# Kernel optimization log

Measured on AMD Instinct MI355X. Metric: run time of the kernel, lower is better.

## Reference

```python
import jax, jax.numpy as jnp
import numpy as np
from jax import lax

E, H, I, K, T = 16, 2048, 1408, 2, 8192


def setup_inputs() -> dict:
    key = jax.random.key(0)
    k1, k2, k3, k4, k5 = jax.random.split(key, 5)
    hidden_states = jax.random.normal(k1, (T, H), dtype=jnp.float32)
    top_k_index = jax.random.randint(k2, (T, K), 0, E, dtype=jnp.int64)
    top_k_weights = jax.random.uniform(k3, (T, K), dtype=jnp.float32)
    gate_up_proj = jax.random.normal(k4, (E, 2 * I, H), dtype=jnp.float32) * 0.02
    down_proj = jax.random.normal(k5, (E, H, I), dtype=jnp.float32) * 0.02
    return {
        "hidden_states": hidden_states,
        "top_k_index": top_k_index,
        "top_k_weights": top_k_weights,
        "gate_up_proj": gate_up_proj,
        "down_proj": down_proj,
    }


def _moe_forward(hidden_states, top_k_index, top_k_weights, gate_up_proj, down_proj):
    # Combine weight per (expert, token): sum over top-k slots where the slot
    # routes to that expert. Tokens not routed to an expert get weight 0, so the
    # dense per-expert GEMM below computes the exact same math as the gather/
    # scatter-add loop in the original module (masking is linear post-GEMM).
    one_hot = jax.nn.one_hot(top_k_index, E, dtype=top_k_weights.dtype)  # [T,K,E]
    combine = jnp.einsum("tke,tk->et", one_hot, top_k_weights)           # [E,T]

    def expert_step(acc, xs):
        w_gu, w_d, cw = xs                      # [2I,H], [H,I], [T]
        gu = hidden_states @ w_gu.T             # [T,2I]
        gate, up = jnp.split(gu, 2, axis=-1)    # chunk(2, dim=-1)
        h = jax.nn.silu(gate) * up              # SwiGLU
        out = h @ w_d.T                         # [T,H]
        return acc + out * cw[:, None], None

    acc0 = jnp.zeros_like(hidden_states)
    final, _ = lax.scan(expert_step, acc0, (gate_up_proj, down_proj, combine))
    return final


def reference(hidden_states, top_k_index, top_k_weights, gate_up_proj, down_proj):
    return _moe_forward(hidden_states, top_k_index, top_k_weights, gate_up_proj, down_proj)
```

## Files before the change

### kernel.cpp

```cpp
#include <hip/hip_runtime.h>
#include <hip/hip_bf16.h>

#define E_ 16
#define H_ 2048
#define I_ 1408
#define TWOI_ 2816
#define K_ 2
#define T_ 8192
#define TK_ 16384

typedef unsigned short ushort_t;
typedef unsigned int uint_t;
typedef short short8 __attribute__((ext_vector_type(8)));
typedef float f32x4 __attribute__((ext_vector_type(4)));

#define AS1 __attribute__((address_space(1)))
#define AS3 __attribute__((address_space(3)))

__device__ __forceinline__ void gl2lds16(const ushort_t* g, ushort_t* l) {
    __builtin_amdgcn_global_load_lds((const AS1 uint_t*)g, (AS3 uint_t*)l, 16, 0, 0);
}

__device__ __forceinline__ ushort_t f2bf(float f) {
    uint_t u = __float_as_uint(f);
    u += 0x7fffu + ((u >> 16) & 1u);
    return (ushort_t)(u >> 16);
}
__device__ __forceinline__ uint_t pack2(float a, float b) {
    return (uint_t)f2bf(a) | ((uint_t)f2bf(b) << 16);
}
__device__ __forceinline__ float bflo(uint_t v) { return __uint_as_float(v << 16); }
__device__ __forceinline__ float bfhi(uint_t v) { return __uint_as_float(v & 0xffff0000u); }

__global__ void routing_kernel(const int* __restrict__ idx32,
                               const float* __restrict__ wts,
                               int* __restrict__ meta,
                               int* __restrict__ token_ids,
                               float* __restrict__ slot_w) {
    __shared__ int s_cnt[E_], s_off[E_ + 1], s_cur[E_], s_orodd;
    const int tid = threadIdx.x;
    if (tid < E_) { s_cnt[tid] = 0; s_cur[tid] = 0; }
    if (tid == 0) s_orodd = 0;
    __syncthreads();
    int ao = 0;
    for (int s = tid; s < TK_ / 2; s += (int)blockDim.x) ao |= idx32[2 * s + 1];
    atomicOr(&s_orodd, ao);
    __syncthreads();
    const bool is64 = (s_orodd == 0);
    for (int s = tid; s < TK_; s += (int)blockDim.x) {
        int e = is64 ? idx32[2 * s] : idx32[s];
        atomicAdd(&s_cnt[e], 1);
    }
    __syncthreads();
    if (tid == 0) {
        int acc = 0, nt = 0;
        for (int e = 0; e < E_; e++) {
            s_off[e] = acc;
            meta[1 + e] = acc;
            for (int m = 0; m < s_cnt[e]; m += 128) {
                meta[32 + nt] = e;
                meta[192 + nt] = acc + m;
                nt++;
            }
            acc += s_cnt[e];
        }
        s_off[E_] = acc;
        meta[1 + E_] = acc;
        meta[0] = nt;
    }
    __syncthreads();
    for (int s = tid; s < TK_; s += (int)blockDim.x) {
        int e = is64 ? idx32[2 * s] : idx32[s];
        int p = atomicAdd(&s_cur[e], 1);
        int r = s_off[e] + p;
        token_ids[r] = s >> 1;
        slot_w[r] = wts[s];
    }
}

__global__ void f2bf_kernel(const float* __restrict__ src, ushort_t* __restrict__ dst, int n8) {
    int i = blockIdx.x * blockDim.x + threadIdx.x;
    const int stride = gridDim.x * blockDim.x;
    for (; i < n8; i += stride) {
        const float4* s = (const float4*)src + 2 * (size_t)i;
        float4 a = s[0], b = s[1];
        uint4 o;
        o.x = pack2(a.x, a.y);
        o.y = pack2(a.z, a.w);
        o.z = pack2(b.x, b.y);
        o.w = pack2(b.z, b.w);
        ((uint4*)dst)[i] = o;
    }
}

__global__ void swiglu_kernel(const ushort_t* __restrict__ GU, ushort_t* __restrict__ Hb) {
    const int n8 = TK_ * (I_ / 8);
    int i = blockIdx.x * blockDim.x + threadIdx.x;
    const int stride = gridDim.x * blockDim.x;
    for (; i < n8; i += stride) {
        int r = i / (I_ / 8);
        int c = (i % (I_ / 8)) * 8;
        const uint4 gv = *(const uint4*)(GU + (size_t)r * TWOI_ + c);
        const uint4 uv = *(const uint4*)(GU + (size_t)r * TWOI_ + I_ + c);
        const uint_t gs[4] = {gv.x, gv.y, gv.z, gv.w};
        const uint_t us[4] = {uv.x, uv.y, uv.z, uv.w};
        uint_t o[4];
#pragma unroll
        for (int j = 0; j < 4; j++) {
            float g0 = bflo(gs[j]), g1 = bfhi(gs[j]);
            float u0 = bflo(us[j]), u1 = bfhi(us[j]);
            float h0 = g0 / (1.f + __expf(-g0)) * u0;
            float h1 = g1 / (1.f + __expf(-g1)) * u1;
            o[j] = pack2(h0, h1);
        }
        *(uint4*)(Hb + (size_t)r * I_ + c) = make_uint4(o[0], o[1], o[2], o[3]);
    }
}

template <int NCOLS, int KDIM, int MODE>
__global__ __launch_bounds__(256) void moe_gemm(
    const ushort_t* __restrict__ A, const ushort_t* __restrict__ Bw,
    const int* __restrict__ meta, const int* __restrict__ token_ids,
    const float* __restrict__ slot_w, ushort_t* __restrict__ GU,
    float* __restrict__ Out) {
    __shared__ ushort_t As[128 * 32];
    __shared__ ushort_t Bs[128 * 32];
    const int bx = blockIdx.x;
    if (bx >= meta[0]) return;
    const int e = meta[32 + bx];
    const int row0 = meta[192 + bx];
    const int rend = meta[1 + e + 1];
    const int mrows = min(128, rend - row0);
    const int n0 = blockIdx.y * 128;
    const int tid = threadIdx.x;
    const int lane = tid & 63, wid = tid >> 6;
    const int wr = wid >> 1, wc = wid & 1;

    const int c0 = wid * 2, c1 = wid * 2 + 1;
    const int ra0 = c0 * 16 + (lane >> 2);
    const int ra1 = c1 * 16 + (lane >> 2);
    const int kc = (lane & 3) * 8;
    const int rg0 = row0 + min(ra0, mrows - 1);
    const int rg1 = row0 + min(ra1, mrows - 1);
    const long arow0 = (MODE == 0) ? (long)token_ids[rg0] : (long)rg0;
    const long arow1 = (MODE == 0) ? (long)token_ids[rg1] : (long)rg1;
    const ushort_t* ap0 = A + arow0 * KDIM + kc;
    const ushort_t* ap1 = A + arow1 * KDIM + kc;
    const ushort_t* Be = Bw + (size_t)e * NCOLS * KDIM;
    const ushort_t* bp0 = Be + (size_t)(n0 + ra0) * KDIM + kc;
    const ushort_t* bp1 = Be + (size_t)(n0 + ra1) * KDIM + kc;
    ushort_t* as0 = As + c0 * 512;
    ushort_t* as1 = As + c1 * 512;
    ushort_t* bs0 = Bs + c0 * 512;
    ushort_t* bs1 = Bs + c1 * 512;

    f32x4 acc[4][4];
#pragma unroll
    for (int i = 0; i < 4; i++)
#pragma unroll
        for (int j = 0; j < 4; j++) acc[i][j] = (f32x4){0.f, 0.f, 0.f, 0.f};

    for (int k = 0; k < KDIM; k += 32) {
        __syncthreads();
        gl2lds16(ap0, as0);
        gl2lds16(ap1, as1);
        gl2lds16(bp0, bs0);
        gl2lds16(bp1, bs1);
        ap0 += 32; ap1 += 32; bp0 += 32; bp1 += 32;
        __syncthreads();
        short8 af[4], bf[4];
        const int fr = lane & 15, fq = (lane >> 4) * 8;
#pragma unroll
        for (int mt = 0; mt < 4; mt++)
            af[mt] = *(const short8*)(As + (wr * 64 + mt * 16 + fr) * 32 + fq);
#pragma unroll
        for (int nt = 0; nt < 4; nt++)
            bf[nt] = *(const short8*)(Bs + (wc * 64 + nt * 16 + fr) * 32 + fq);
#pragma unroll
        for (int mt = 0; mt < 4; mt++)
#pragma unroll
            for (int nt = 0; nt < 4; nt++)
                acc[mt][nt] = __builtin_amdgcn_mfma_f32_16x16x32_bf16(af[mt], bf[nt], acc[mt][nt], 0, 0, 0);
    }

    const int quad = lane >> 4, tn = lane & 15;
    if (MODE == 0) {
#pragma unroll
        for (int mt = 0; mt < 4; mt++) {
#pragma unroll
            for (int reg = 0; reg < 4; reg++) {
                const int rl = wr * 64 + mt * 16 + quad * 4 + reg;
                if (rl < mrows) {
                    ushort_t* dst = GU + (size_t)(row0 + rl) * NCOLS + n0 + wc * 64 + tn;
#pragma unroll
                    for (int nt = 0; nt < 4; nt++) dst[nt * 16] = f2bf(acc[mt][nt][reg]);
                }
            }
        }
    } else {
#pragma unroll
        for (int mt = 0; mt < 4; mt++) {
#pragma unroll
            for (int reg = 0; reg < 4; reg++) {
                const int rl = wr * 64 + mt * 16 + quad * 4 + reg;
                if (rl < mrows) {
                    const int row = row0 + rl;
                    const int t = token_ids[row];
                    const float w = slot_w[row];
                    float* dst = Out + (size_t)t * NCOLS + n0 + wc * 64 + tn;
#pragma unroll
                    for (int nt = 0; nt < 4; nt++) atomicAdd(dst + nt * 16, acc[mt][nt][reg] * w);
                }
            }
        }
    }
}

extern "C" void kernel_launch(void* const* d_in, const int* in_sizes, int n_in,
                              void* d_out, int out_size, void* d_ws, size_t ws_size,
                              hipStream_t stream) {
    const float* hidden = (const float*)d_in[0];
    const int* topk_idx = (const int*)d_in[1];
    const float* topk_w = (const float*)d_in[2];
    const float* w_gu = (const float*)d_in[3];
    const float* w_d = (const float*)d_in[4];
    float* out = (float*)d_out;

    char* ws = (char*)d_ws;
    int* meta = (int*)ws;
    int* token_ids = (int*)(ws + 4096);
    float* slot_w = (float*)(ws + 4096 + 65536);
    ushort_t* Xb = (ushort_t*)(ws + 135168);
    ushort_t* Wgu = Xb + (size_t)T_ * H_;
    ushort_t* Wd = Wgu + (size_t)E_ * TWOI_ * H_;
    ushort_t* GU = Wd + (size_t)E_ * H_ * I_;
    ushort_t* Hb = GU + (size_t)TK_ * TWOI_;

    hipMemsetAsync(d_out, 0, (size_t)out_size * sizeof(float), stream);

    routing_kernel<<<1, 1024, 0, stream>>>(topk_idx, topk_w, meta, token_ids, slot_w);

    f2bf_kernel<<<4096, 256, 0, stream>>>(hidden, Xb, (int)((size_t)T_ * H_ / 8));
    f2bf_kernel<<<8192, 256, 0, stream>>>(w_gu, Wgu, (int)((size_t)E_ * TWOI_ * H_ / 8));
    f2bf_kernel<<<8192, 256, 0, stream>>>(w_d, Wd, (int)((size_t)E_ * H_ * I_ / 8));

    moe_gemm<TWOI_, H_, 0><<<dim3(144, 22), 256, 0, stream>>>(
        Xb, Wgu, meta, token_ids, slot_w, GU, out);

    swiglu_kernel<<<4096, 256, 0, stream>>>(GU, Hb);

    moe_gemm<H_, I_, 1><<<dim3(144, 16), 256, 0, stream>>>(
        Hb, Wd, meta, token_ids, slot_w, GU, out);
}
```

Baseline: 1.299 ms.

## Fuse SwiGLU into gate-up GEMM epilogue and replace atomic scatter with combine kernel

Gate/up weight rows are interleaved in 16-row groups during bf16 conversion, so each GEMM tile holds matching gate and up columns and applies SwiGLU in its epilogue. This removes the separate swiglu pass and the full GU intermediate. The down GEMM now writes bf16 per-slot rows, and a combine kernel gathers the two slots per token with their weights, replacing fp32 atomicAdd scatter and the output memset. A grouped block-index swizzle is also added for L2 reuse. The cost is an extra Y buffer pass plus bf16 rounding of the down-projection output before weighting.

```diff
diff --git a/kernel.cpp b/kernel.cpp
--- a/kernel.cpp
+++ b/kernel.cpp
@@ -36,7 +36,7 @@
                                const float* __restrict__ wts,
                                int* __restrict__ meta,
                                int* __restrict__ token_ids,
-                               float* __restrict__ slot_w) {
+                               int* __restrict__ row_of_slot) {
     __shared__ int s_cnt[E_], s_off[E_ + 1], s_cur[E_], s_orodd;
     const int tid = threadIdx.x;
     if (tid < E_) { s_cnt[tid] = 0; s_cur[tid] = 0; }
@@ -74,7 +74,7 @@
         int p = atomicAdd(&s_cur[e], 1);
         int r = s_off[e] + p;
         token_ids[r] = s >> 1;
-        slot_w[r] = wts[s];
+        row_of_slot[s] = r;
     }
 }
 
@@ -93,27 +93,27 @@
     }
 }
 
-__global__ void swiglu_kernel(const ushort_t* __restrict__ GU, ushort_t* __restrict__ Hb) {
-    const int n8 = TK_ * (I_ / 8);
+__global__ void f2bf_gu_kernel(const float* __restrict__ src, ushort_t* __restrict__ dst) {
+    const int PER_E = TWOI_ * (H_ / 8);
+    const int n8 = E_ * PER_E;
     int i = blockIdx.x * blockDim.x + threadIdx.x;
     const int stride = gridDim.x * blockDim.x;
     for (; i < n8; i += stride) {
-        int r = i / (I_ / 8);
-        int c = (i % (I_ / 8)) * 8;
-        const uint4 gv = *(const uint4*)(GU + (size_t)r * TWOI_ + c);
-        const uint4 uv = *(const uint4*)(GU + (size_t)r * TWOI_ + I_ + c);
-        const uint_t gs[4] = {gv.x, gv.y, gv.z, gv.w};
-        const uint_t us[4] = {uv.x, uv.y, uv.z, uv.w};
-        uint_t o[4];
-#pragma unroll
-        for (int j = 0; j < 4; j++) {
-            float g0 = bflo(gs[j]), g1 = bfhi(gs[j]);
-            float u0 = bflo(us[j]), u1 = bfhi(us[j]);
-            float h0 = g0 / (1.f + __expf(-g0)) * u0;
-            float h1 = g1 / (1.f + __expf(-g1)) * u1;
-            o[j] = pack2(h0, h1);
-        }
-        *(uint4*)(Hb + (size_t)r * I_ + c) = make_uint4(o[0], o[1], o[2], o[3]);
+        int e = i / PER_E;
+        int rem = i % PER_E;
+        int r = rem / (H_ / 8);
+        int cg = rem % (H_ / 8);
+        int pr;
+        if (r < I_) pr = 32 * (r >> 4) + (r & 15);
+        else { int r2 = r - I_; pr = 32 * (r2 >> 4) + 16 + (r2 & 15); }
+        const float4* s = (const float4*)src + 2 * (size_t)i;
+        float4 a = s[0], b = s[1];
+        uint4 o;
+        o.x = pack2(a.x, a.y);
+        o.y = pack2(a.z, a.w);
+        o.z = pack2(b.x, b.y);
+        o.w = pack2(b.z, b.w);
+        *(uint4*)(dst + ((size_t)e * TWOI_ + pr) * H_ + cg * 8) = o;
     }
 }
 
@@ -121,17 +121,25 @@
 __global__ __launch_bounds__(256) void moe_gemm(
     const ushort_t* __restrict__ A, const ushort_t* __restrict__ Bw,
     const int* __restrict__ meta, const int* __restrict__ token_ids,
-    const float* __restrict__ slot_w, ushort_t* __restrict__ GU,
-    float* __restrict__ Out) {
+    ushort_t* __restrict__ Obf) {
     __shared__ ushort_t As[128 * 32];
     __shared__ ushort_t Bs[128 * 32];
-    const int bx = blockIdx.x;
-    if (bx >= meta[0]) return;
+    const int ny = NCOLS / 128;
+    const int nx = meta[0];
+    const int flat = blockIdx.x;
+    if (flat >= nx * ny) return;
+    const int GROUP = 8;
+    const int gid = flat / (GROUP * ny);
+    const int rem = flat % (GROUP * ny);
+    const int gx = min(GROUP, nx - gid * GROUP);
+    const int bx = gid * GROUP + rem % gx;
+    const int by = rem / gx;
+
     const int e = meta[32 + bx];
     const int row0 = meta[192 + bx];
     const int rend = meta[1 + e + 1];
     const int mrows = min(128, rend - row0);
-    const int n0 = blockIdx.y * 128;
+    const int n0 = by * 128;
     const int tid = threadIdx.x;
     const int lane = tid & 63, wid = tid >> 6;
     const int wr = wid >> 1, wc = wid & 1;
@@ -185,34 +193,65 @@
 
     const int quad = lane >> 4, tn = lane & 15;
     if (MODE == 0) {
+        const int hbase = ((n0 + wc * 64) >> 1) + tn;
 #pragma unroll
         for (int mt = 0; mt < 4; mt++) {
 #pragma unroll
             for (int reg = 0; reg < 4; reg++) {
                 const int rl = wr * 64 + mt * 16 + quad * 4 + reg;
                 if (rl < mrows) {
-                    ushort_t* dst = GU + (size_t)(row0 + rl) * NCOLS + n0 + wc * 64 + tn;
+                    ushort_t* dst = Obf + (size_t)(row0 + rl) * I_ + hbase;
+#pragma unroll
+                    for (int j = 0; j < 2; j++) {
+                        float g = acc[mt][2 * j][reg];
+                        float u = acc[mt][2 * j + 1][reg];
+                        float h = g / (1.f + __expf(-g)) * u;
+                        dst[j * 16] = f2bf(h);
+                    }
+                }
+            }
+        }
+    } else {
+#pragma unroll
+        for (int mt = 0; mt < 4; mt++) {
+#pragma unroll
+            for (int reg = 0; reg < 4; reg++) {
+                const int rl = wr * 64 + mt * 16 + quad * 4 + reg;
+                if (rl < mrows) {
+                    ushort_t* dst = Obf + (size_t)(row0 + rl) * NCOLS + n0 + wc * 64 + tn;
 #pragma unroll
                     for (int nt = 0; nt < 4; nt++) dst[nt * 16] = f2bf(acc[mt][nt][reg]);
                 }
             }
         }
-    } else {
-#pragma unroll
-        for (int mt = 0; mt < 4; mt++) {
-#pragma unroll
-            for (int reg = 0; reg < 4; reg++) {
-                const int rl = wr * 64 + mt * 16 + quad * 4 + reg;
-                if (rl < mrows) {
-                    const int row = row0 + rl;
-                    const int t = token_ids[row];
-                    const float w = slot_w[row];
-                    float* dst = Out + (size_t)t * NCOLS + n0 + wc * 64 + tn;
-#pragma unroll
-                    for (int nt = 0; nt < 4; nt++) atomicAdd(dst + nt * 16, acc[mt][nt][reg] * w);
-                }
-            }
-        }
+    }
+}
+
+__global__ void combine_kernel(const ushort_t* __restrict__ Y,
+                               const int* __restrict__ row_of_slot,
+                               const float* __restrict__ wts,
+                               float* __restrict__ out) {
+    const int n8 = T_ * (H_ / 8);
+    int i = blockIdx.x * blockDim.x + threadIdx.x;
+    const int stride = gridDim.x * blockDim.x;
+    for (; i < n8; i += stride) {
+        const int t = i / (H_ / 8);
+        const int c = (i % (H_ / 8)) * 8;
+        const int r0 = row_of_slot[2 * t], r1 = row_of_slot[2 * t + 1];
+        const float w0 = wts[2 * t], w1 = wts[2 * t + 1];
+        const uint4 y0 = *(const uint4*)(Y + (size_t)r0 * H_ + c);
+        const uint4 y1 = *(const uint4*)(Y + (size_t)r1 * H_ + c);
+        const uint_t a[4] = {y0.x, y0.y, y0.z, y0.w};
+        const uint_t b[4] = {y1.x, y1.y, y1.z, y1.w};
+        float o[8];
+#pragma unroll
+        for (int j = 0; j < 4; j++) {
+            o[2 * j]     = w0 * bflo(a[j]) + w1 * bflo(b[j]);
+            o[2 * j + 1] = w0 * bfhi(a[j]) + w1 * bfhi(b[j]);
+        }
+        float4* dst = (float4*)(out + (size_t)t * H_ + c);
+        dst[0] = make_float4(o[0], o[1], o[2], o[3]);
+        dst[1] = make_float4(o[4], o[5], o[6], o[7]);
     }
 }
 
@@ -229,26 +268,24 @@
     char* ws = (char*)d_ws;
     int* meta = (int*)ws;
     int* token_ids = (int*)(ws + 4096);
-    float* slot_w = (float*)(ws + 4096 + 65536);
+    int* row_of_slot = (int*)(ws + 4096 + 65536);
     ushort_t* Xb = (ushort_t*)(ws + 135168);
     ushort_t* Wgu = Xb + (size_t)T_ * H_;
     ushort_t* Wd = Wgu + (size_t)E_ * TWOI_ * H_;
-    ushort_t* GU = Wd + (size_t)E_ * H_ * I_;
-    ushort_t* Hb = GU + (size_t)TK_ * TWOI_;
-
-    hipMemsetAsync(d_out, 0, (size_t)out_size * sizeof(float), stream);
-
-    routing_kernel<<<1, 1024, 0, stream>>>(topk_idx, topk_w, meta, token_ids, slot_w);
+    ushort_t* Hb = Wd + (size_t)E_ * H_ * I_;
+    ushort_t* Y = Hb + (size_t)TK_ * I_;
+
+    routing_kernel<<<1, 1024, 0, stream>>>(topk_idx, topk_w, meta, token_ids, row_of_slot);
 
     f2bf_kernel<<<4096, 256, 0, stream>>>(hidden, Xb, (int)((size_t)T_ * H_ / 8));
-    f2bf_kernel<<<8192, 256, 0, stream>>>(w_gu, Wgu, (int)((size_t)E_ * TWOI_ * H_ / 8));
+    f2bf_gu_kernel<<<8192, 256, 0, stream>>>(w_gu, Wgu);
     f2bf_kernel<<<8192, 256, 0, stream>>>(w_d, Wd, (int)((size_t)E_ * H_ * I_ / 8));
 
-    moe_gemm<TWOI_, H_, 0><<<dim3(144, 22), 256, 0, stream>>>(
-        Xb, Wgu, meta, token_ids, slot_w, GU, out);
-
-    swiglu_kernel<<<4096, 256, 0, stream>>>(GU, Hb);
-
-    moe_gemm<H_, I_, 1><<<dim3(144, 16), 256, 0, stream>>>(
-        Hb, Wd, meta, token_ids, slot_w, GU, out);
-}
+    moe_gemm<TWOI_, H_, 0><<<144 * 22, 256, 0, stream>>>(
+        Xb, Wgu, meta, token_ids, Hb);
+
+    moe_gemm<H_, I_, 1><<<144 * 16, 256, 0, stream>>>(
+        Hb, Wd, meta, token_ids, Y);
+
+    combine_kernel<<<4096, 256, 0, stream>>>(Y, row_of_slot, topk_w, out);
+}
```

Measured after the change: 1.121 ms. -13.7%, faster.
